# Kernel tuning notes

Hardware: AMD Instinct MI355X
Metric: run time of the kernel (lower is better)

The kernel has to match this reference:

```python
import jax, jax.numpy as jnp
import numpy as np

N, F_IN, H, C, E, K = 100000, 128, 512, 16, 3200000, 3
EPS = 1e-5


def setup_inputs() -> dict:
    key = jax.random.key(0)
    ks = jax.random.split(key, 12)
    x = jax.random.normal(ks[0], (N, F_IN), jnp.float32)
    edge_index = jax.random.randint(ks[1], (2, E), 0, N, jnp.int64)
    # TAGConv has K+1 hop linears (bias folded into one vector, like PyG)
    W1 = jax.random.normal(ks[2], (K + 1, F_IN, H), jnp.float32) * 0.02
    b1 = jnp.zeros((H,), jnp.float32)
    W2 = jax.random.normal(ks[3], (K + 1, H, H), jnp.float32) * 0.02
    b2 = jnp.zeros((H,), jnp.float32)
    W3 = jax.random.normal(ks[4], (K + 1, H, C), jnp.float32) * 0.02
    b3 = jnp.zeros((C,), jnp.float32)
    gn1_w = jnp.ones((H,), jnp.float32)
    gn1_b = jnp.zeros((H,), jnp.float32)
    gn1_a = jnp.ones((H,), jnp.float32)  # mean_scale alpha
    gn2_w = jnp.ones((H,), jnp.float32)
    gn2_b = jnp.zeros((H,), jnp.float32)
    gn2_a = jnp.ones((H,), jnp.float32)
    return {"x": x, "edge_index": edge_index,
            "W1": W1, "b1": b1, "W2": W2, "b2": b2, "W3": W3, "b3": b3,
            "gn1_w": gn1_w, "gn1_b": gn1_b, "gn1_a": gn1_a,
            "gn2_w": gn2_w, "gn2_b": gn2_b, "gn2_a": gn2_a}


def _gcn_norm(edge_index, n):
    # PyG TAGConv: gcn_norm with add_self_loops=False, all-ones edge weights
    row, col = edge_index[0], edge_index[1]  # source j, target i
    deg = jax.ops.segment_sum(jnp.ones((edge_index.shape[1],), jnp.float32), col,
                              num_segments=n)
    dinv = jnp.where(deg > 0, jax.lax.rsqrt(jnp.maximum(deg, 1.0)), 0.0)
    return row, col, dinv[row] * dinv[col]


def _prop(h, row, col, norm, n):
    # out[i] = sum_{(j->i)} norm_e * h[j]
    return jax.ops.segment_sum(norm[:, None] * h[row], col, num_segments=n)


def _tagconv(x, row, col, norm, W, b):
    n = x.shape[0]
    out = x @ W[0]
    h = x
    for k in range(1, W.shape[0]):
        h = _prop(h, row, col, norm, n)
        out = out + h @ W[k]
    return out + b


def _graphnorm(x, w, b, a):
    # single graph: per-graph mean/var over all nodes
    mean = jnp.mean(x, axis=0)
    sub = x - a * mean
    var = jnp.mean(sub * sub, axis=0)
    return sub * jax.lax.rsqrt(var + EPS) * w + b


def reference(x, edge_index, W1, b1, W2, b2, W3, b3,
              gn1_w, gn1_b, gn1_a, gn2_w, gn2_b, gn2_a):
    n = x.shape[0]
    row, col, norm = _gcn_norm(edge_index, n)
    h = jax.nn.relu(_tagconv(x, row, col, norm, W1, b1))
    h = _graphnorm(h, gn1_w, gn1_b, gn1_a)
    h = jax.nn.relu(_tagconv(h, row, col, norm, W2, b2))
    h = _graphnorm(h, gn2_w, gn2_b, gn2_a)
    return _tagconv(h, row, col, norm, W3, b3)
```

## Files before the change

kernel.cpp:

```cpp
#include <hip/hip_runtime.h>

#define NN 100000
#define EE 3200000
#define EPSF 1e-5f

typedef unsigned short u16;
typedef short bf16x8 __attribute__((ext_vector_type(8)));
typedef float f32x4 __attribute__((ext_vector_type(4)));

static inline int cdiv(int a, int b) { return (a + b - 1) / b; }

__device__ __forceinline__ float b2f(u16 u) {
    return __uint_as_float((unsigned int)u << 16);
}
__device__ __forceinline__ u16 f2b(float f) {
    unsigned int i = __float_as_uint(f);
    return (u16)((i + 0x7FFFu + ((i >> 16) & 1u)) >> 16);
}
__device__ __forceinline__ int ep_src(unsigned int p) { return (int)(p & 0x1FFFFu); }
__device__ __forceinline__ float ep_w(unsigned int p) {
    return __uint_as_float(p & 0xFFFE0000u);
}
__device__ __forceinline__ unsigned pkhi(float f0, float f1) {
    return __builtin_amdgcn_perm(__float_as_uint(f1), __float_as_uint(f0), 0x07060302u);
}

__global__ void k_init(int* __restrict__ deg, int* __restrict__ cursor,
                       float* __restrict__ stats) {
    int i = blockIdx.x * 256 + threadIdx.x;
    if (i < NN) {
        deg[i] = 0;
        cursor[i] = 0;
    }
    if (i < 2048) stats[i] = 0.f;
}

__global__ void k_deg(const int* __restrict__ col, int* __restrict__ deg) {
    int i = blockIdx.x * 256 + threadIdx.x;
    if (i < EE) atomicAdd(&deg[col[i]], 1);
}

__global__ void k_dinv(const int* __restrict__ deg, float* __restrict__ dinv) {
    int i = blockIdx.x * 256 + threadIdx.x;
    if (i < NN) {
        int d = deg[i];
        dinv[i] = d > 0 ? rsqrtf((float)d) : 0.f;
    }
}

__global__ void k_scan(const int* __restrict__ deg, int* __restrict__ offs) {
    __shared__ int sh[1024];
    int tid = threadIdx.x;
    int start = tid * 98;
    int end = min(start + 98, NN);
    int sum = 0;
    for (int i = start; i < end; ++i) sum += deg[i];
    sh[tid] = sum;
    __syncthreads();
    for (int off = 1; off < 1024; off <<= 1) {
        int t = (tid >= off) ? sh[tid - off] : 0;
        __syncthreads();
        sh[tid] += t;
        __syncthreads();
    }
    int base = tid ? sh[tid - 1] : 0;
    for (int i = start; i < end; ++i) {
        offs[i] = base;
        base += deg[i];
    }
    if (tid == 1023) offs[NN] = sh[1023];
}

__global__ void k_scatter(const int* __restrict__ row, const int* __restrict__ col,
                          const float* __restrict__ dinv, const int* __restrict__ offs,
                          int* __restrict__ cursor, unsigned int* __restrict__ ep) {
    int i = blockIdx.x * 256 + threadIdx.x;
    if (i < EE) {
        int c = col[i], r = row[i];
        int pos = offs[c] + atomicAdd(&cursor[c], 1);
        float w = dinv[r] * dinv[c];
        unsigned int u = __float_as_uint(w);
        unsigned int rb = (u + 0xFFFFu + ((u >> 17) & 1u)) & 0xFFFE0000u;
        ep[pos] = rb | (unsigned int)r;
    }
}

__global__ void k_cvt(const float* __restrict__ src, u16* __restrict__ dst, int n4) {
    int idx = blockIdx.x * 256 + threadIdx.x;
    if (idx >= n4) return;
    float4 v = ((const float4*)src)[idx];
    ushort4 o;
    o.x = f2b(v.x);
    o.y = f2b(v.y);
    o.z = f2b(v.z);
    o.w = f2b(v.w);
    ((ushort4*)dst)[idx] = o;
}

__global__ void k_cvt8s(const u16* __restrict__ src, int lds_, unsigned char* __restrict__ dst,
                        int ldd) {
    int idx = blockIdx.x * 256 + threadIdx.x;
    if (idx >= NN * 128) return;
    int node = idx >> 7, f2 = (idx & 127) << 1;
    ushort2 v = *(const ushort2*)(src + (size_t)node * lds_ + f2);
    int pk = __builtin_amdgcn_cvt_pk_fp8_f32(b2f(v.x), b2f(v.y), 0, false);
    uchar2 o;
    o.x = (unsigned char)(pk & 0xFF);
    o.y = (unsigned char)((pk >> 8) & 0xFF);
    *(uchar2*)(dst + (size_t)node * ldd + f2) = o;
}

template <int S8>
__global__ void k_prop_t(const void* __restrict__ in, int ldin,
                         unsigned char* __restrict__ out8, int ldo8,
                         const int* __restrict__ offs, const unsigned int* __restrict__ ep) {
    int node = blockIdx.x;
    int f2 = threadIdx.x << 1;
    int s = offs[node], e = offs[node + 1];
    const u16* inb = (const u16*)in;
    const unsigned char* in8 = (const unsigned char*)in;
    float a0 = 0.f, a1 = 0.f;
    int t = s;
    for (; t + 4 <= e; t += 4) {
        unsigned int p0 = ep[t], p1 = ep[t + 1], p2 = ep[t + 2], p3 = ep[t + 3];
        float x0, y0, x1, y1, x2, y2, x3, y3;
        if (S8) {
            uchar2 c0 = *(const uchar2*)(in8 + (size_t)ep_src(p0) * ldin + f2);
            uchar2 c1 = *(const uchar2*)(in8 + (size_t)ep_src(p1) * ldin + f2);
            uchar2 c2 = *(const uchar2*)(in8 + (size_t)ep_src(p2) * ldin + f2);
            uchar2 c3 = *(const uchar2*)(in8 + (size_t)ep_src(p3) * ldin + f2);
            int w0 = c0.x | (c0.y << 8), w1 = c1.x | (c1.y << 8);
            int w2 = c2.x | (c2.y << 8), w3 = c3.x | (c3.y << 8);
            x0 = __builtin_amdgcn_cvt_f32_fp8(w0, 0);
            y0 = __builtin_amdgcn_cvt_f32_fp8(w0, 1);
            x1 = __builtin_amdgcn_cvt_f32_fp8(w1, 0);
            y1 = __builtin_amdgcn_cvt_f32_fp8(w1, 1);
            x2 = __builtin_amdgcn_cvt_f32_fp8(w2, 0);
            y2 = __builtin_amdgcn_cvt_f32_fp8(w2, 1);
            x3 = __builtin_amdgcn_cvt_f32_fp8(w3, 0);
            y3 = __builtin_amdgcn_cvt_f32_fp8(w3, 1);
        } else {
            ushort2 v0 = *(const ushort2*)(inb + (size_t)ep_src(p0) * ldin + f2);
            ushort2 v1 = *(const ushort2*)(inb + (size_t)ep_src(p1) * ldin + f2);
            ushort2 v2 = *(const ushort2*)(inb + (size_t)ep_src(p2) * ldin + f2);
            ushort2 v3 = *(const ushort2*)(inb + (size_t)ep_src(p3) * ldin + f2);
            x0 = b2f(v0.x);
            y0 = b2f(v0.y);
            x1 = b2f(v1.x);
            y1 = b2f(v1.y);
            x2 = b2f(v2.x);
            y2 = b2f(v2.y);
            x3 = b2f(v3.x);
            y3 = b2f(v3.y);
        }
        float w0 = ep_w(p0), w1 = ep_w(p1), w2 = ep_w(p2), w3 = ep_w(p3);
        a0 = fmaf(w0, x0, a0);
        a1 = fmaf(w0, y0, a1);
        a0 = fmaf(w1, x1, a0);
        a1 = fmaf(w1, y1, a1);
        a0 = fmaf(w2, x2, a0);
        a1 = fmaf(w2, y2, a1);
        a0 = fmaf(w3, x3, a0);
        a1 = fmaf(w3, y3, a1);
    }
    for (; t < e; ++t) {
        unsigned int p0 = ep[t];
        float x0, y0;
        if (S8) {
            uchar2 c0 = *(const uchar2*)(in8 + (size_t)ep_src(p0) * ldin + f2);
            int w = c0.x | (c0.y << 8);
            x0 = __builtin_amdgcn_cvt_f32_fp8(w, 0);
            y0 = __builtin_amdgcn_cvt_f32_fp8(w, 1);
        } else {
            ushort2 v0 = *(const ushort2*)(inb + (size_t)ep_src(p0) * ldin + f2);
            x0 = b2f(v0.x);
            y0 = b2f(v0.y);
        }
        float w0 = ep_w(p0);
        a0 = fmaf(w0, x0, a0);
        a1 = fmaf(w0, y0, a1);
    }
    int pk = __builtin_amdgcn_cvt_pk_fp8_f32(a0, a1, 0, false);
    uchar2 o8;
    o8.x = (unsigned char)(pk & 0xFF);
    o8.y = (unsigned char)((pk >> 8) & 0xFF);
    *(uchar2*)(out8 + (size_t)node * ldo8 + f2) = o8;
}

__global__ void k_prop256(const unsigned char* __restrict__ in, int ldin,
                          unsigned char* __restrict__ out, int ldout,
                          const int* __restrict__ offs, const unsigned int* __restrict__ ep) {
    int node = blockIdx.x;
    int f4 = threadIdx.x << 2;
    int s = offs[node], e = offs[node + 1];
    float a0 = 0, a1 = 0, a2 = 0, a3 = 0;
    int t = s;
    for (; t + 4 <= e; t += 4) {
        unsigned int p[4];
        unsigned int v[4];
#pragma unroll
        for (int u = 0; u < 4; ++u) p[u] = ep[t + u];
#pragma unroll
        for (int u = 0; u < 4; ++u)
            v[u] = *(const unsigned int*)(in + (size_t)ep_src(p[u]) * ldin + f4);
#pragma unroll
        for (int u = 0; u < 4; ++u) {
            float w = ep_w(p[u]);
            a0 = fmaf(w, __builtin_amdgcn_cvt_f32_fp8((int)v[u], 0), a0);
            a1 = fmaf(w, __builtin_amdgcn_cvt_f32_fp8((int)v[u], 1), a1);
            a2 = fmaf(w, __builtin_amdgcn_cvt_f32_fp8((int)v[u], 2), a2);
            a3 = fmaf(w, __builtin_amdgcn_cvt_f32_fp8((int)v[u], 3), a3);
        }
    }
    for (; t < e; ++t) {
        unsigned int p0 = ep[t];
        unsigned int v = *(const unsigned int*)(in + (size_t)ep_src(p0) * ldin + f4);
        float w = ep_w(p0);
        a0 = fmaf(w, __builtin_amdgcn_cvt_f32_fp8((int)v, 0), a0);
        a1 = fmaf(w, __builtin_amdgcn_cvt_f32_fp8((int)v, 1), a1);
        a2 = fmaf(w, __builtin_amdgcn_cvt_f32_fp8((int)v, 2), a2);
        a3 = fmaf(w, __builtin_amdgcn_cvt_f32_fp8((int)v, 3), a3);
    }
    int p01 = __builtin_amdgcn_cvt_pk_fp8_f32(a0, a1, 0, false);
    int p23 = __builtin_amdgcn_cvt_pk_fp8_f32(a2, a3, 0, false);
    unsigned int o = (unsigned)(p01 & 0xFFFF) | ((unsigned)p23 << 16);
    *(unsigned int*)(out + (size_t)node * ldout + f4) = o;
}

__global__ void k_prop16(const float* __restrict__ in, int ldin,
                         const float* __restrict__ add, int ldadd,
                         float* __restrict__ out, const float* __restrict__ bias,
                         const int* __restrict__ offs, const unsigned int* __restrict__ ep) {
    int node = blockIdx.x * 16 + (threadIdx.x >> 4);
    if (node >= NN) return;
    int f = threadIdx.x & 15;
    float acc = add[(size_t)node * ldadd + f];
    int s = offs[node], e = offs[node + 1];
    int t = s;
    for (; t + 8 <= e; t += 8) {
        unsigned int p[8];
        float v[8];
#pragma unroll
        for (int u = 0; u < 8; ++u) p[u] = ep[t + u];
#pragma unroll
        for (int u = 0; u < 8; ++u) v[u] = in[(size_t)ep_src(p[u]) * ldin + f];
#pragma unroll
        for (int u = 0; u < 8; ++u) acc = fmaf(ep_w(p[u]), v[u], acc);
    }
    for (; t < e; ++t) {
        unsigned int p0 = ep[t];
        acc = fmaf(ep_w(p0), in[(size_t)ep_src(p0) * ldin + f], acc);
    }
    if (bias) acc += bias[f];
    out[node * 16 + f] = acc;
}

__device__ __forceinline__ void stage_bf16(char* lds, const char* src, size_t rowB,
                                           int colOff, int rowBase, int rowMax, int tid) {
    int wave = tid >> 6, lane = tid & 63;
#pragma unroll
    for (int i = 0; i < 2; ++i) {
        int L = i * 4096 + wave * 1024 + lane * 16;
        int r = L >> 6;
        int kog = (L & 63) ^ ((r & 3) << 4);
        int gr = rowBase + r;
        if (gr > rowMax) gr = rowMax;
        const char* g = src + (size_t)gr * rowB + colOff + kog;
        __builtin_amdgcn_global_load_lds(
            (const __attribute__((address_space(1))) void*)g,
            (__attribute__((address_space(3))) void*)(lds + i * 4096 + wave * 1024), 16, 0, 0);
    }
}

__global__ __launch_bounds__(256) void k_gemm_mfma(
    const void* __restrict__ A0, int lda0, const void* __restrict__ A1, int lda1,
    const void* __restrict__ A2, int lda2, const void* __restrict__ A3, int lda3, int a8mask,
    const u16* __restrict__ B0, const u16* __restrict__ B1, const u16* __restrict__ B2,
    const u16* __restrict__ B3, int ldb, void* __restrict__ Cv, int ldc, int M, int Ncols,
    int Ktot, int Kq, const float* __restrict__ bias, int relu, int cmode,
    float* __restrict__ statsOut) {
    __shared__ __align__(16) u16 As[128 * 32];
    __shared__ __align__(16) u16 Bs[128 * 32];
    __shared__ float sstat[256];
    char* AsB = (char*)As;
    char* BsB = (char*)Bs;
    int tid = threadIdx.x;
    int wave = tid >> 6, lane = tid & 63;
    int quad = lane >> 4, lq = lane & 15;
    int wr = wave >> 1, wc = wave & 1;
    int m0 = blockIdx.y * 128, n0 = blockIdx.x * 128;
    f32x4 acc[4][4] = {};
    if (statsOut) sstat[tid] = 0.f;

    int src = 0, kk = 0;
    for (int ks = 0; ks < Ktot; ks += 32) {
        const void* Ap = src == 0 ? A0 : src == 1 ? A1 : src == 2 ? A2 : A3;
        int lda = src == 0 ? lda0 : src == 1 ? lda1 : src == 2 ? lda2 : lda3;
        const u16* Bp = src == 0 ? B0 : src == 1 ? B1 : src == 2 ? B2 : B3;
        if ((a8mask >> src) & 1) {
            const unsigned char* A8 = (const unsigned char*)Ap;
            int r = tid >> 1, h = tid & 1;
            int gr = m0 + r;
            if (gr > M - 1) gr = M - 1;
            uint4 wv = *(const uint4*)(A8 + (size_t)gr * lda + kk + h * 16);
            uint4 lo, hi;
            lo.x = pkhi(__builtin_amdgcn_cvt_f32_fp8((int)wv.x, 0),
                        __builtin_amdgcn_cvt_f32_fp8((int)wv.x, 1));
            lo.y = pkhi(__builtin_amdgcn_cvt_f32_fp8((int)wv.x, 2),
                        __builtin_amdgcn_cvt_f32_fp8((int)wv.x, 3));
            lo.z = pkhi(__builtin_amdgcn_cvt_f32_fp8((int)wv.y, 0),
                        __builtin_amdgcn_cvt_f32_fp8((int)wv.y, 1));
            lo.w = pkhi(__builtin_amdgcn_cvt_f32_fp8((int)wv.y, 2),
                        __builtin_amdgcn_cvt_f32_fp8((int)wv.y, 3));
            hi.x = pkhi(__builtin_amdgcn_cvt_f32_fp8((int)wv.z, 0),
                        __builtin_amdgcn_cvt_f32_fp8((int)wv.z, 1));
            hi.y = pkhi(__builtin_amdgcn_cvt_f32_fp8((int)wv.z, 2),
                        __builtin_amdgcn_cvt_f32_fp8((int)wv.z, 3));
            hi.z = pkhi(__builtin_amdgcn_cvt_f32_fp8((int)wv.w, 0),
                        __builtin_amdgcn_cvt_f32_fp8((int)wv.w, 1));
            hi.w = pkhi(__builtin_amdgcn_cvt_f32_fp8((int)wv.w, 2),
                        __builtin_amdgcn_cvt_f32_fp8((int)wv.w, 3));
            int s = (r & 3) << 4;
            *(uint4*)(AsB + r * 64 + ((h * 32) ^ s)) = lo;
            *(uint4*)(AsB + r * 64 + ((h * 32 + 16) ^ s)) = hi;
        } else {
            stage_bf16(AsB, (const char*)Ap, (size_t)lda * 2, kk * 2, m0, M - 1, tid);
        }
        stage_bf16(BsB, (const char*)Bp, (size_t)ldb * 2, kk * 2, n0, Ncols - 1, tid);
        __syncthreads();
        bf16x8 af[4], bfr[4];
#pragma unroll
        for (int i = 0; i < 4; ++i) {
            int r = wr * 64 + i * 16 + lq;
            af[i] = *(bf16x8*)(AsB + r * 64 + ((quad * 16) ^ ((r & 3) << 4)));
        }
#pragma unroll
        for (int j = 0; j < 4; ++j) {
            int n = wc * 64 + j * 16 + lq;
            bfr[j] = *(bf16x8*)(BsB + n * 64 + ((quad * 16) ^ ((n & 3) << 4)));
        }
#pragma unroll
        for (int i = 0; i < 4; ++i)
#pragma unroll
            for (int j = 0; j < 4; ++j)
                acc[i][j] = __builtin_amdgcn_mfma_f32_16x16x32_bf16(af[i], bfr[j], acc[i][j],
                                                                    0, 0, 0);
        __syncthreads();
        kk += 32;
        if (kk == Kq) {
            kk = 0;
            ++src;
        }
    }

#pragma unroll
    for (int i = 0; i < 4; ++i) {
#pragma unroll
        for (int j = 0; j < 4; ++j) {
            int jc = wc * 64 + j * 16 + lq;
            int c = n0 + jc;
            bool cok = c < Ncols;
            float bcol = (bias && cok) ? bias[c] : 0.f;
            int rbase = m0 + wr * 64 + i * 16 + quad * 4;
            float ls = 0.f, lq2 = 0.f;
#pragma unroll
            for (int reg = 0; reg < 4; ++reg) {
                int r = rbase + reg;
                if (r >= M || !cok) continue;
                float t = acc[i][j][reg];
                if (cmode == 2) t += b2f(*((u16*)Cv + (size_t)r * ldc + c));
                t += bcol;
                if (relu) t = fmaxf(t, 0.f);
                if (cmode == 0)
                    ((float*)Cv)[(size_t)r * ldc + c] = t;
                else
                    *((u16*)Cv + (size_t)r * ldc + c) = f2b(t);
                ls += t;
                lq2 += t * t;
            }
            if (statsOut && cok) {
                atomicAdd(&sstat[jc], ls);
                atomicAdd(&sstat[128 + jc], lq2);
            }
        }
    }
    if (statsOut) {
        __syncthreads();
        if (tid < 128)
            atomicAdd(&statsOut[n0 + tid], sstat[tid]);
        else
            atomicAdd(&statsOut[512 + n0 + (tid - 128)], sstat[tid]);
    }
}

__global__ void k_gnorm(u16* __restrict__ X, int ld, const float* __restrict__ stats,
                        const float* __restrict__ w, const float* __restrict__ b,
                        const float* __restrict__ a) {
    int i = blockIdx.x;
    int c = threadIdx.x * 2;
    const float invn = 1.f / NN;
    ushort2 v = *(ushort2*)(X + (size_t)i * ld + c);
    float x0 = b2f(v.x), x1 = b2f(v.y);
    {
        float m = stats[c] * invn, q = stats[512 + c] * invn, al = a[c];
        float var = q - (2.f * al - al * al) * m * m;
        x0 = (x0 - al * m) * rsqrtf(var + EPSF) * w[c] + b[c];
    }
    {
        int c1 = c + 1;
        float m = stats[c1] * invn, q = stats[512 + c1] * invn, al = a[c1];
        float var = q - (2.f * al - al * al) * m * m;
        x1 = (x1 - al * m) * rsqrtf(var + EPSF) * w[c1] + b[c1];
    }
    v.x = f2b(x0);
    v.y = f2b(x1);
    *(ushort2*)(X + (size_t)i * ld + c) = v;
}

__global__ void k_wt(const float* __restrict__ src, u16* __restrict__ dst, int I, int O,
                     int total) {
    int idx = blockIdx.x * 256 + threadIdx.x;
    if (idx >= total) return;
    int io = I * O;
    int k = idx / io, rem = idx - k * io;
    int n = rem / I, i = rem - n * I;
    dst[idx] = f2b(src[(size_t)k * io + (size_t)i * O + n]);
}

__global__ void k_wt3(const float* __restrict__ W3, u16* __restrict__ W3T) {
    int idx = blockIdx.x * 256 + threadIdx.x;
    if (idx >= 64 * 512) return;
    int n = idx >> 9, i = idx & 511;
    int k = n >> 4, f = n & 15;
    W3T[idx] = f2b(W3[((size_t)k * 512 + i) * 16 + f]);
}

extern "C" void kernel_launch(void* const* d_in, const int* in_sizes, int n_in,
                              void* d_out, int out_size, void* d_ws, size_t ws_size,
                              hipStream_t stream) {
    const float* x = (const float*)d_in[0];
    const int* ei = (const int*)d_in[1];
    const float* W1 = (const float*)d_in[2];
    const float* b1 = (const float*)d_in[3];
    const float* W2 = (const float*)d_in[4];
    const float* b2 = (const float*)d_in[5];
    const float* W3 = (const float*)d_in[6];
    const float* b3 = (const float*)d_in[7];
    const float* g1w = (const float*)d_in[8];
    const float* g1b = (const float*)d_in[9];
    const float* g1a = (const float*)d_in[10];
    const float* g2w = (const float*)d_in[11];
    const float* g2b = (const float*)d_in[12];
    const float* g2a = (const float*)d_in[13];
    const int* row = ei;
    const int* col = ei + EE;

    char* p = (char*)d_ws;
    auto alloc = [&](size_t bytes) {
        char* r = p;
        p += (bytes + 255) & ~(size_t)255;
        return r;
    };
    u16* H1 = (u16*)alloc((size_t)NN * 512 * 2);
    u16* Y = (u16*)alloc((size_t)NN * 512 * 2);
    unsigned char* X8 = (unsigned char*)alloc((size_t)NN * 256);
    unsigned int* ep = (unsigned int*)alloc((size_t)EE * 4);
    u16* W1T = (u16*)alloc((size_t)4 * 512 * 128 * 2);
    u16* W2T = (u16*)alloc((size_t)4 * 512 * 512 * 2);
    u16* W3T = (u16*)alloc(64 * 512 * 2);
    float* dinv = (float*)alloc((size_t)NN * 4);
    float* stats = (float*)alloc(2048 * 4);
    int* deg = (int*)alloc((size_t)NN * 4);
    int* offs = (int*)alloc((size_t)(NN + 1) * 4);
    int* cursor = (int*)alloc((size_t)NN * 4);
    (void)ws_size;
    (void)in_sizes;
    (void)n_in;
    (void)out_size;

    u16* xb = Y;
    unsigned char* F8a = (unsigned char*)Y + (size_t)NN * 256;
    unsigned char* F8b = (unsigned char*)Y + (size_t)NN * 256 + (size_t)NN * 128;

    k_init<<<cdiv(NN, 256), 256, 0, stream>>>(deg, cursor, stats);
    k_deg<<<cdiv(EE, 256), 256, 0, stream>>>(col, deg);
    k_dinv<<<cdiv(NN, 256), 256, 0, stream>>>(deg, dinv);
    k_scan<<<1, 1024, 0, stream>>>(deg, offs);
    k_scatter<<<cdiv(EE, 256), 256, 0, stream>>>(row, col, dinv, offs, cursor, ep);
    k_wt<<<cdiv(4 * 128 * 512, 256), 256, 0, stream>>>(W1, W1T, 128, 512, 4 * 128 * 512);
    k_wt<<<cdiv(4 * 512 * 512, 256), 256, 0, stream>>>(W2, W2T, 512, 512, 4 * 512 * 512);
    k_wt3<<<cdiv(64 * 512, 256), 256, 0, stream>>>(W3, W3T);

    dim3 gg(512 / 128, cdiv(NN, 128));
    const size_t WQ = (size_t)512 * 512;
    const size_t W1Q = (size_t)512 * 128;

    k_cvt<<<cdiv(NN * 32, 256), 256, 0, stream>>>(x, xb, NN * 32);
    k_prop_t<0><<<NN, 64, 0, stream>>>(xb, 128, F8a, 128, offs, ep);
    k_gemm_mfma<<<gg, 256, 0, stream>>>(xb, 128, F8a, 128, xb, 128, xb, 128, 2, W1T,
                                        W1T + W1Q, W1T, W1T, 128, H1, 512, NN, 512, 256, 128,
                                        nullptr, 0, 1, nullptr);
    k_prop_t<1><<<NN, 64, 0, stream>>>(F8a, 128, F8b, 128, offs, ep);
    k_prop_t<1><<<NN, 64, 0, stream>>>(F8b, 128, F8a, 128, offs, ep);
    k_gemm_mfma<<<gg, 256, 0, stream>>>(F8b, 128, F8a, 128, xb, 128, xb, 128, 3,
                                        W1T + 2 * W1Q, W1T + 3 * W1Q, W1T, W1T, 128, H1, 512,
                                        NN, 512, 256, 128, b1, 1, 2, stats);
    k_gnorm<<<NN, 256, 0, stream>>>(H1, 512, stats, g1w, g1b, g1a);

    for (int c = 0; c < 2; ++c) {
        u16* h1c = H1 + 256 * c;
        k_cvt8s<<<cdiv(NN * 128, 256), 256, 0, stream>>>(h1c, 512, X8, 256);
        k_gemm_mfma<<<gg, 256, 0, stream>>>(h1c, 512, h1c, 512, h1c, 512, h1c, 512, 0,
                                            W2T + 256 * c, W2T, W2T, W2T, 512, Y, 512, NN, 512,
                                            256, 256, nullptr, 0, c == 0 ? 1 : 2, nullptr);
        unsigned char* hp1 = (unsigned char*)H1 + 512 * c;
        unsigned char* hp2 = hp1 + 256;
        k_prop256<<<NN, 64, 0, stream>>>(X8, 256, hp1, 1024, offs, ep);
        k_prop256<<<NN, 64, 0, stream>>>(hp1, 1024, hp2, 1024, offs, ep);
        k_prop256<<<NN, 64, 0, stream>>>(hp2, 1024, X8, 256, offs, ep);
        k_gemm_mfma<<<gg, 256, 0, stream>>>(hp1, 1024, hp2, 1024, X8, 256, X8, 256, 7,
                                            W2T + WQ + 256 * c, W2T + 2 * WQ + 256 * c,
                                            W2T + 3 * WQ + 256 * c, W2T, 512, Y, 512, NN, 512,
                                            768, 256, (c == 1) ? b2 : nullptr, c == 1 ? 1 : 0,
                                            2, (c == 1) ? (stats + 1024) : nullptr);
    }
    k_gnorm<<<NN, 256, 0, stream>>>(Y, 512, stats + 1024, g2w, g2b, g2a);

    float* G = (float*)H1;
    float* tA = (float*)X8;
    float* tB = tA + (size_t)NN * 16;
    {
        dim3 g3(1, cdiv(NN, 128));
        k_gemm_mfma<<<g3, 256, 0, stream>>>(Y, 512, Y, 512, Y, 512, Y, 512, 0, W3T, W3T, W3T,
                                            W3T, 512, G, 64, NN, 64, 512, 512, nullptr, 0, 0,
                                            nullptr);
    }
    k_prop16<<<cdiv(NN, 16), 256, 0, stream>>>(G + 48, 64, G + 32, 64, tA, nullptr, offs, ep);
    k_prop16<<<cdiv(NN, 16), 256, 0, stream>>>(tA, 16, G + 16, 64, tB, nullptr, offs, ep);
    k_prop16<<<cdiv(NN, 16), 256, 0, stream>>>(tB, 16, G + 0, 64, (float*)d_out, b3, offs, ep);
}
```

Baseline: 2.776 ms.

## Double-buffer GEMM LDS tiles, remap workgroups per XCD, merge hop GEMMs

The MFMA GEMM now uses double-buffered LDS. The next B tile is prefetched with global_load_lds and the next A tile is loaded into registers, with explicit waitcnts and one barrier per K step in place of two syncthreads. Blocks are remapped so consecutive tiles land on the same XCD, the LDS swizzle changes, and launch bounds request higher occupancy. On the host side, the layer-1 hop GEMMs and the second layer-2 chunk GEMMs are fused into single launches over all four hop sources. This cuts launches and the read-modify-write of the output, at the cost of more registers and LDS per block.

```diff
diff --git a/kernel.cpp b/kernel.cpp
--- a/kernel.cpp
+++ b/kernel.cpp
@@ -255,89 +255,134 @@
     out[node * 16 + f] = acc;
 }
 
-__device__ __forceinline__ void stage_bf16(char* lds, const char* src, size_t rowB,
-                                           int colOff, int rowBase, int rowMax, int tid) {
-    int wave = tid >> 6, lane = tid & 63;
-#pragma unroll
-    for (int i = 0; i < 2; ++i) {
-        int L = i * 4096 + wave * 1024 + lane * 16;
-        int r = L >> 6;
-        int kog = (L & 63) ^ ((r & 3) << 4);
-        int gr = rowBase + r;
-        if (gr > rowMax) gr = rowMax;
-        const char* g = src + (size_t)gr * rowB + colOff + kog;
-        __builtin_amdgcn_global_load_lds(
-            (const __attribute__((address_space(1))) void*)g,
-            (__attribute__((address_space(3))) void*)(lds + i * 4096 + wave * 1024), 16, 0, 0);
-    }
-}
-
-__global__ __launch_bounds__(256) void k_gemm_mfma(
+__global__ __launch_bounds__(256, 4) void k_gemm_mfma(
     const void* __restrict__ A0, int lda0, const void* __restrict__ A1, int lda1,
     const void* __restrict__ A2, int lda2, const void* __restrict__ A3, int lda3, int a8mask,
     const u16* __restrict__ B0, const u16* __restrict__ B1, const u16* __restrict__ B2,
     const u16* __restrict__ B3, int ldb, void* __restrict__ Cv, int ldc, int M, int Ncols,
     int Ktot, int Kq, const float* __restrict__ bias, int relu, int cmode,
     float* __restrict__ statsOut) {
-    __shared__ __align__(16) u16 As[128 * 32];
-    __shared__ __align__(16) u16 Bs[128 * 32];
+    __shared__ __align__(16) char AsB[2][8192];
+    __shared__ __align__(16) char BsB[2][8192];
     __shared__ float sstat[256];
-    char* AsB = (char*)As;
-    char* BsB = (char*)Bs;
     int tid = threadIdx.x;
     int wave = tid >> 6, lane = tid & 63;
     int quad = lane >> 4, lq = lane & 15;
     int wr = wave >> 1, wc = wave & 1;
-    int m0 = blockIdx.y * 128, n0 = blockIdx.x * 128;
+    int gx = gridDim.x;
+    int nwg = gx * (int)gridDim.y;
+    int lin = blockIdx.y * gx + blockIdx.x;
+    int xcd = lin & 7, kk8 = lin >> 3;
+    int q8 = nwg >> 3, r8 = nwg & 7;
+    int wgid = (xcd < r8 ? xcd * (q8 + 1) : r8 * (q8 + 1) + (xcd - r8) * q8) + kk8;
+    int m0 = (wgid / gx) * 128, n0 = (wgid % gx) * 128;
+    int r = tid >> 1, h = tid & 1;
+    int gr = m0 + r;
+    if (gr > M - 1) gr = M - 1;
     f32x4 acc[4][4] = {};
     if (statsOut) sstat[tid] = 0.f;
 
-    int src = 0, kk = 0;
-    for (int ks = 0; ks < Ktot; ks += 32) {
-        const void* Ap = src == 0 ? A0 : src == 1 ? A1 : src == 2 ? A2 : A3;
+    const int NT = Ktot >> 5;
+    const int spm = (Kq >> 5) - 1;
+    const int sps = __popc(spm);
+
+    auto loadA = [&](int u, uint4& x0, uint4& x1, int& t8) {
+        int sU = u < NT ? u : NT - 1;
+        int src = sU >> sps, kk = (sU & spm) << 5;
+        const char* Ap = (const char*)(src == 0 ? A0 : src == 1 ? A1 : src == 2 ? A2 : A3);
         int lda = src == 0 ? lda0 : src == 1 ? lda1 : src == 2 ? lda2 : lda3;
+        t8 = (a8mask >> src) & 1;
+        if (t8) {
+            x0 = *(const uint4*)(Ap + (size_t)gr * lda + kk + h * 16);
+        } else {
+            const char* base = Ap + (size_t)gr * ((size_t)lda * 2) + (size_t)kk * 2 + h * 32;
+            x0 = *(const uint4*)base;
+            x1 = *(const uint4*)(base + 16);
+        }
+    };
+    auto writeA = [&](int buf, uint4 x0, uint4 x1, int t8) {
+        uint4 lo, hi;
+        if (t8) {
+            lo.x = pkhi(__builtin_amdgcn_cvt_f32_fp8((int)x0.x, 0),
+                        __builtin_amdgcn_cvt_f32_fp8((int)x0.x, 1));
+            lo.y = pkhi(__builtin_amdgcn_cvt_f32_fp8((int)x0.x, 2),
+                        __builtin_amdgcn_cvt_f32_fp8((int)x0.x, 3));
+            lo.z = pkhi(__builtin_amdgcn_cvt_f32_fp8((int)x0.y, 0),
+                        __builtin_amdgcn_cvt_f32_fp8((int)x0.y, 1));
+            lo.w = pkhi(__builtin_amdgcn_cvt_f32_fp8((int)x0.y, 2),
+                        __builtin_amdgcn_cvt_f32_fp8((int)x0.y, 3));
+            hi.x = pkhi(__builtin_amdgcn_cvt_f32_fp8((int)x0.z, 0),
+                        __builtin_amdgcn_cvt_f32_fp8((int)x0.z, 1));
+            hi.y = pkhi(__builtin_amdgcn_cvt_f32_fp8((int)x0.z, 2),
+                        __builtin_amdgcn_cvt_f32_fp8((int)x0.z, 3));
+            hi.z = pkhi(__builtin_amdgcn_cvt_f32_fp8((int)x0.w, 0),
+                        __builtin_amdgcn_cvt_f32_fp8((int)x0.w, 1));
+            hi.w = pkhi(__builtin_amdgcn_cvt_f32_fp8((int)x0.w, 2),
+                        __builtin_amdgcn_cvt_f32_fp8((int)x0.w, 3));
+        } else {
+            lo = x0;
+            hi = x1;
+        }
+        int s = ((r >> 1) & 3) << 4;
+        char* dst = AsB[buf] + r * 64;
+        *(uint4*)(dst + ((h * 32) ^ s)) = lo;
+        *(uint4*)(dst + ((h * 32 + 16) ^ s)) = hi;
+    };
+    auto stageB = [&](int buf, int u) {
+        int sU = u < NT ? u : NT - 1;
+        int src = sU >> sps, kk = (sU & spm) << 5;
         const u16* Bp = src == 0 ? B0 : src == 1 ? B1 : src == 2 ? B2 : B3;
-        if ((a8mask >> src) & 1) {
-            const unsigned char* A8 = (const unsigned char*)Ap;
-            int r = tid >> 1, h = tid & 1;
-            int gr = m0 + r;
-            if (gr > M - 1) gr = M - 1;
-            uint4 wv = *(const uint4*)(A8 + (size_t)gr * lda + kk + h * 16);
-            uint4 lo, hi;
-            lo.x = pkhi(__builtin_amdgcn_cvt_f32_fp8((int)wv.x, 0),
-                        __builtin_amdgcn_cvt_f32_fp8((int)wv.x, 1));
-            lo.y = pkhi(__builtin_amdgcn_cvt_f32_fp8((int)wv.x, 2),
-                        __builtin_amdgcn_cvt_f32_fp8((int)wv.x, 3));
-            lo.z = pkhi(__builtin_amdgcn_cvt_f32_fp8((int)wv.y, 0),
-                        __builtin_amdgcn_cvt_f32_fp8((int)wv.y, 1));
-            lo.w = pkhi(__builtin_amdgcn_cvt_f32_fp8((int)wv.y, 2),
-                        __builtin_amdgcn_cvt_f32_fp8((int)wv.y, 3));
-            hi.x = pkhi(__builtin_amdgcn_cvt_f32_fp8((int)wv.z, 0),
-                        __builtin_amdgcn_cvt_f32_fp8((int)wv.z, 1));
-            hi.y = pkhi(__builtin_amdgcn_cvt_f32_fp8((int)wv.z, 2),
-                        __builtin_amdgcn_cvt_f32_fp8((int)wv.z, 3));
-            hi.z = pkhi(__builtin_amdgcn_cvt_f32_fp8((int)wv.w, 0),
-                        __builtin_amdgcn_cvt_f32_fp8((int)wv.w, 1));
-            hi.w = pkhi(__builtin_amdgcn_cvt_f32_fp8((int)wv.w, 2),
-                        __builtin_amdgcn_cvt_f32_fp8((int)wv.w, 3));
-            int s = (r & 3) << 4;
-            *(uint4*)(AsB + r * 64 + ((h * 32) ^ s)) = lo;
-            *(uint4*)(AsB + r * 64 + ((h * 32 + 16) ^ s)) = hi;
-        } else {
-            stage_bf16(AsB, (const char*)Ap, (size_t)lda * 2, kk * 2, m0, M - 1, tid);
-        }
-        stage_bf16(BsB, (const char*)Bp, (size_t)ldb * 2, kk * 2, n0, Ncols - 1, tid);
-        __syncthreads();
+#pragma unroll
+        for (int i = 0; i < 2; ++i) {
+            int L = i * 4096 + wave * 1024 + lane * 16;
+            int rr = L >> 6;
+            int kog = (L & 63) ^ (((rr >> 1) & 3) << 4);
+            int gn = n0 + rr;
+            if (gn > Ncols - 1) gn = Ncols - 1;
+            const char* g = (const char*)Bp + (size_t)gn * ((size_t)ldb * 2) +
+                            (size_t)kk * 2 + kog;
+            __builtin_amdgcn_global_load_lds(
+                (const __attribute__((address_space(1))) void*)g,
+                (__attribute__((address_space(3))) void*)(BsB[buf] + i * 4096 + wave * 1024),
+                16, 0, 0);
+        }
+    };
+
+    uint4 pa0, pa1;
+    int pt8;
+    {
+        uint4 a0_, a1_;
+        int t8_;
+        loadA(0, a0_, a1_, t8_);
+        stageB(0, 0);
+        asm volatile("s_waitcnt vmcnt(2)" ::: "memory");
+        __builtin_amdgcn_sched_barrier(0);
+        writeA(0, a0_, a1_, t8_);
+        loadA(1, pa0, pa1, pt8);
+        if (pt8)
+            asm volatile("s_waitcnt vmcnt(1) lgkmcnt(0)" ::: "memory");
+        else
+            asm volatile("s_waitcnt vmcnt(2) lgkmcnt(0)" ::: "memory");
+        __builtin_amdgcn_sched_barrier(0);
+        __builtin_amdgcn_s_barrier();
+    }
+
+    int cur = 0;
+    for (int t = 0; t < NT; ++t) {
+        int nxt = cur ^ 1;
+        stageB(nxt, t + 1);
+        const char* Ac = AsB[cur];
+        const char* Bc = BsB[cur];
         bf16x8 af[4], bfr[4];
 #pragma unroll
         for (int i = 0; i < 4; ++i) {
-            int r = wr * 64 + i * 16 + lq;
-            af[i] = *(bf16x8*)(AsB + r * 64 + ((quad * 16) ^ ((r & 3) << 4)));
+            int rr = wr * 64 + i * 16 + lq;
+            af[i] = *(const bf16x8*)(Ac + rr * 64 + ((quad * 16) ^ (((rr >> 1) & 3) << 4)));
         }
 #pragma unroll
         for (int j = 0; j < 4; ++j) {
-            int n = wc * 64 + j * 16 + lq;
-            bfr[j] = *(bf16x8*)(BsB + n * 64 + ((quad * 16) ^ ((n & 3) << 4)));
+            int nn2 = wc * 64 + j * 16 + lq;
+            bfr[j] = *(const bf16x8*)(Bc + nn2 * 64 + ((quad * 16) ^ (((nn2 >> 1) & 3) << 4)));
         }
 #pragma unroll
         for (int i = 0; i < 4; ++i)
@@ -345,12 +390,17 @@
             for (int j = 0; j < 4; ++j)
                 acc[i][j] = __builtin_amdgcn_mfma_f32_16x16x32_bf16(af[i], bfr[j], acc[i][j],
                                                                     0, 0, 0);
-        __syncthreads();
-        kk += 32;
-        if (kk == Kq) {
-            kk = 0;
-            ++src;
-        }
+        asm volatile("s_waitcnt vmcnt(2)" ::: "memory");
+        __builtin_amdgcn_sched_barrier(0);
+        writeA(nxt, pa0, pa1, pt8);
+        loadA(t + 2, pa0, pa1, pt8);
+        if (pt8)
+            asm volatile("s_waitcnt vmcnt(1) lgkmcnt(0)" ::: "memory");
+        else
+            asm volatile("s_waitcnt vmcnt(2) lgkmcnt(0)" ::: "memory");
+        __builtin_amdgcn_sched_barrier(0);
+        __builtin_amdgcn_s_barrier();
+        cur = nxt;
     }
 
 #pragma unroll
@@ -365,16 +415,16 @@
             float ls = 0.f, lq2 = 0.f;
 #pragma unroll
             for (int reg = 0; reg < 4; ++reg) {
-                int r = rbase + reg;
-                if (r >= M || !cok) continue;
+                int rr = rbase + reg;
+                if (rr >= M || !cok) continue;
                 float t = acc[i][j][reg];
-                if (cmode == 2) t += b2f(*((u16*)Cv + (size_t)r * ldc + c));
+                if (cmode == 2) t += b2f(*((u16*)Cv + (size_t)rr * ldc + c));
                 t += bcol;
                 if (relu) t = fmaxf(t, 0.f);
                 if (cmode == 0)
-                    ((float*)Cv)[(size_t)r * ldc + c] = t;
+                    ((float*)Cv)[(size_t)rr * ldc + c] = t;
                 else
-                    *((u16*)Cv + (size_t)r * ldc + c) = f2b(t);
+                    *((u16*)Cv + (size_t)rr * ldc + c) = f2b(t);
                 ls += t;
                 lq2 += t * t;
             }
@@ -497,32 +547,39 @@
 
     k_cvt<<<cdiv(NN * 32, 256), 256, 0, stream>>>(x, xb, NN * 32);
     k_prop_t<0><<<NN, 64, 0, stream>>>(xb, 128, F8a, 128, offs, ep);
-    k_gemm_mfma<<<gg, 256, 0, stream>>>(xb, 128, F8a, 128, xb, 128, xb, 128, 2, W1T,
-                                        W1T + W1Q, W1T, W1T, 128, H1, 512, NN, 512, 256, 128,
-                                        nullptr, 0, 1, nullptr);
     k_prop_t<1><<<NN, 64, 0, stream>>>(F8a, 128, F8b, 128, offs, ep);
-    k_prop_t<1><<<NN, 64, 0, stream>>>(F8b, 128, F8a, 128, offs, ep);
-    k_gemm_mfma<<<gg, 256, 0, stream>>>(F8b, 128, F8a, 128, xb, 128, xb, 128, 3,
-                                        W1T + 2 * W1Q, W1T + 3 * W1Q, W1T, W1T, 128, H1, 512,
-                                        NN, 512, 256, 128, b1, 1, 2, stats);
+    k_prop_t<1><<<NN, 64, 0, stream>>>(F8b, 128, X8, 128, offs, ep);
+    k_gemm_mfma<<<gg, 256, 0, stream>>>(xb, 128, F8a, 128, F8b, 128, X8, 128, 14, W1T,
+                                        W1T + W1Q, W1T + 2 * W1Q, W1T + 3 * W1Q, 128, H1, 512,
+                                        NN, 512, 512, 128, b1, 1, 1, stats);
     k_gnorm<<<NN, 256, 0, stream>>>(H1, 512, stats, g1w, g1b, g1a);
 
-    for (int c = 0; c < 2; ++c) {
-        u16* h1c = H1 + 256 * c;
-        k_cvt8s<<<cdiv(NN * 128, 256), 256, 0, stream>>>(h1c, 512, X8, 256);
-        k_gemm_mfma<<<gg, 256, 0, stream>>>(h1c, 512, h1c, 512, h1c, 512, h1c, 512, 0,
-                                            W2T + 256 * c, W2T, W2T, W2T, 512, Y, 512, NN, 512,
-                                            256, 256, nullptr, 0, c == 0 ? 1 : 2, nullptr);
-        unsigned char* hp1 = (unsigned char*)H1 + 512 * c;
-        unsigned char* hp2 = hp1 + 256;
-        k_prop256<<<NN, 64, 0, stream>>>(X8, 256, hp1, 1024, offs, ep);
-        k_prop256<<<NN, 64, 0, stream>>>(hp1, 1024, hp2, 1024, offs, ep);
-        k_prop256<<<NN, 64, 0, stream>>>(hp2, 1024, X8, 256, offs, ep);
-        k_gemm_mfma<<<gg, 256, 0, stream>>>(hp1, 1024, hp2, 1024, X8, 256, X8, 256, 7,
-                                            W2T + WQ + 256 * c, W2T + 2 * WQ + 256 * c,
-                                            W2T + 3 * WQ + 256 * c, W2T, 512, Y, 512, NN, 512,
-                                            768, 256, (c == 1) ? b2 : nullptr, c == 1 ? 1 : 0,
-                                            2, (c == 1) ? (stats + 1024) : nullptr);
+    unsigned char* hpA = (unsigned char*)H1;
+    unsigned char* hpB = (unsigned char*)H1 + 256;
+    {
+        u16* h1c0 = H1;
+        k_cvt8s<<<cdiv(NN * 128, 256), 256, 0, stream>>>(h1c0, 512, X8, 256);
+        k_gemm_mfma<<<gg, 256, 0, stream>>>(h1c0, 512, h1c0, 512, h1c0, 512, h1c0, 512, 0,
+                                            W2T, W2T, W2T, W2T, 512, Y, 512, NN, 512, 256,
+                                            256, nullptr, 0, 1, nullptr);
+        k_prop256<<<NN, 64, 0, stream>>>(X8, 256, hpA, 1024, offs, ep);
+        k_prop256<<<NN, 64, 0, stream>>>(hpA, 1024, hpB, 1024, offs, ep);
+        k_prop256<<<NN, 64, 0, stream>>>(hpB, 1024, X8, 256, offs, ep);
+        k_gemm_mfma<<<gg, 256, 0, stream>>>(hpA, 1024, hpB, 1024, X8, 256, X8, 256, 7,
+                                            W2T + WQ, W2T + 2 * WQ, W2T + 3 * WQ, W2T, 512,
+                                            Y, 512, NN, 512, 768, 256, nullptr, 0, 2,
+                                            nullptr);
+    }
+    {
+        u16* h1c1 = H1 + 256;
+        k_cvt8s<<<cdiv(NN * 128, 256), 256, 0, stream>>>(h1c1, 512, X8, 256);
+        k_prop256<<<NN, 64, 0, stream>>>(X8, 256, hpA, 1024, offs, ep);
+        k_prop256<<<NN, 64, 0, stream>>>(hpA, 1024, hpB, 1024, offs, ep);
+        k_prop256<<<NN, 64, 0, stream>>>(hpB, 1024, X8, 256, offs, ep);
+        k_gemm_mfma<<<gg, 256, 0, stream>>>(h1c1, 512, hpA, 1024, hpB, 1024, X8, 256, 14,
+                                            W2T + 256, W2T + WQ + 256, W2T + 2 * WQ + 256,
+                                            W2T + 3 * WQ + 256, 512, Y, 512, NN, 512, 1024,
+                                            256, b2, 1, 2, stats + 1024);
     }
     k_gnorm<<<NN, 256, 0, stream>>>(Y, 512, stats + 1024, g2w, g2b, g2a);
 
```

New measurement: 2.988 ms. 1.08x slower.

## Merge TAGConv hop GEMMs into fewer launches, remap workgroups per XCD, widen LDS swizzle

Applied to the files above, without the earlier changes.

Layer 1 now runs all three propagations first and does a single K=512 GEMM over four sources (x and three hops), writing the output once instead of two GEMM passes with a read-modify-write. The second half of layer 2 folds its hop-0 GEMM into the hop GEMM so that half needs one launch. The GEMM kernel also remaps block IDs so consecutive tiles land on the same XCD for L2 locality, replaces the running src/kk counters with shift/mask math, and changes the LDS XOR swizzle to use (r>>1)&3 to reduce bank conflicts. Together these cut GEMM launches and the extra read/write of the bf16 output. The cost is needing an extra fp8 buffer (X8) live during layer 1, and the K-index math assumes Kq is a power of two.

```diff
diff --git a/kernel.cpp b/kernel.cpp
--- a/kernel.cpp
+++ b/kernel.cpp
@@ -262,7 +262,7 @@
     for (int i = 0; i < 2; ++i) {
         int L = i * 4096 + wave * 1024 + lane * 16;
         int r = L >> 6;
-        int kog = (L & 63) ^ ((r & 3) << 4);
+        int kog = (L & 63) ^ (((r >> 1) & 3) << 4);
         int gr = rowBase + r;
         if (gr > rowMax) gr = rowMax;
         const char* g = src + (size_t)gr * rowB + colOff + kog;
@@ -279,21 +279,29 @@
     const u16* __restrict__ B3, int ldb, void* __restrict__ Cv, int ldc, int M, int Ncols,
     int Ktot, int Kq, const float* __restrict__ bias, int relu, int cmode,
     float* __restrict__ statsOut) {
-    __shared__ __align__(16) u16 As[128 * 32];
-    __shared__ __align__(16) u16 Bs[128 * 32];
+    __shared__ __align__(16) char AsB[8192];
+    __shared__ __align__(16) char BsB[8192];
     __shared__ float sstat[256];
-    char* AsB = (char*)As;
-    char* BsB = (char*)Bs;
     int tid = threadIdx.x;
     int wave = tid >> 6, lane = tid & 63;
     int quad = lane >> 4, lq = lane & 15;
     int wr = wave >> 1, wc = wave & 1;
-    int m0 = blockIdx.y * 128, n0 = blockIdx.x * 128;
+    int gx = gridDim.x;
+    int nwg = gx * (int)gridDim.y;
+    int lin = blockIdx.y * gx + blockIdx.x;
+    int xcd = lin & 7, k8 = lin >> 3;
+    int q8 = nwg >> 3, r8 = nwg & 7;
+    int wgid = (xcd < r8 ? xcd * (q8 + 1) : r8 * (q8 + 1) + (xcd - r8) * q8) + k8;
+    int m0 = (wgid / gx) * 128, n0 = (wgid % gx) * 128;
     f32x4 acc[4][4] = {};
     if (statsOut) sstat[tid] = 0.f;
 
-    int src = 0, kk = 0;
-    for (int ks = 0; ks < Ktot; ks += 32) {
+    const int NT = Ktot >> 5;
+    const int spm = (Kq >> 5) - 1;
+    const int sps = __popc(spm);
+
+    for (int t = 0; t < NT; ++t) {
+        int src = t >> sps, kk = (t & spm) << 5;
         const void* Ap = src == 0 ? A0 : src == 1 ? A1 : src == 2 ? A2 : A3;
         int lda = src == 0 ? lda0 : src == 1 ? lda1 : src == 2 ? lda2 : lda3;
         const u16* Bp = src == 0 ? B0 : src == 1 ? B1 : src == 2 ? B2 : B3;
@@ -320,9 +328,10 @@
                         __builtin_amdgcn_cvt_f32_fp8((int)wv.w, 1));
             hi.w = pkhi(__builtin_amdgcn_cvt_f32_fp8((int)wv.w, 2),
                         __builtin_amdgcn_cvt_f32_fp8((int)wv.w, 3));
-            int s = (r & 3) << 4;
-            *(uint4*)(AsB + r * 64 + ((h * 32) ^ s)) = lo;
-            *(uint4*)(AsB + r * 64 + ((h * 32 + 16) ^ s)) = hi;
+            int s = ((r >> 1) & 3) << 4;
+            char* dst = AsB + r * 64;
+            *(uint4*)(dst + ((h * 32) ^ s)) = lo;
+            *(uint4*)(dst + ((h * 32 + 16) ^ s)) = hi;
         } else {
             stage_bf16(AsB, (const char*)Ap, (size_t)lda * 2, kk * 2, m0, M - 1, tid);
         }
@@ -331,13 +340,13 @@
         bf16x8 af[4], bfr[4];
 #pragma unroll
         for (int i = 0; i < 4; ++i) {
-            int r = wr * 64 + i * 16 + lq;
-            af[i] = *(bf16x8*)(AsB + r * 64 + ((quad * 16) ^ ((r & 3) << 4)));
+            int rr = wr * 64 + i * 16 + lq;
+            af[i] = *(const bf16x8*)(AsB + rr * 64 + ((quad * 16) ^ (((rr >> 1) & 3) << 4)));
         }
 #pragma unroll
         for (int j = 0; j < 4; ++j) {
-            int n = wc * 64 + j * 16 + lq;
-            bfr[j] = *(bf16x8*)(BsB + n * 64 + ((quad * 16) ^ ((n & 3) << 4)));
+            int nn2 = wc * 64 + j * 16 + lq;
+            bfr[j] = *(const bf16x8*)(BsB + nn2 * 64 + ((quad * 16) ^ (((nn2 >> 1) & 3) << 4)));
         }
 #pragma unroll
         for (int i = 0; i < 4; ++i)
@@ -346,11 +355,6 @@
                 acc[i][j] = __builtin_amdgcn_mfma_f32_16x16x32_bf16(af[i], bfr[j], acc[i][j],
                                                                     0, 0, 0);
         __syncthreads();
-        kk += 32;
-        if (kk == Kq) {
-            kk = 0;
-            ++src;
-        }
     }
 
 #pragma unroll
@@ -365,16 +369,16 @@
             float ls = 0.f, lq2 = 0.f;
 #pragma unroll
             for (int reg = 0; reg < 4; ++reg) {
-                int r = rbase + reg;
-                if (r >= M || !cok) continue;
+                int rr = rbase + reg;
+                if (rr >= M || !cok) continue;
                 float t = acc[i][j][reg];
-                if (cmode == 2) t += b2f(*((u16*)Cv + (size_t)r * ldc + c));
+                if (cmode == 2) t += b2f(*((u16*)Cv + (size_t)rr * ldc + c));
                 t += bcol;
                 if (relu) t = fmaxf(t, 0.f);
                 if (cmode == 0)
-                    ((float*)Cv)[(size_t)r * ldc + c] = t;
+                    ((float*)Cv)[(size_t)rr * ldc + c] = t;
                 else
-                    *((u16*)Cv + (size_t)r * ldc + c) = f2b(t);
+                    *((u16*)Cv + (size_t)rr * ldc + c) = f2b(t);
                 ls += t;
                 lq2 += t * t;
             }
@@ -497,32 +501,39 @@
 
     k_cvt<<<cdiv(NN * 32, 256), 256, 0, stream>>>(x, xb, NN * 32);
     k_prop_t<0><<<NN, 64, 0, stream>>>(xb, 128, F8a, 128, offs, ep);
-    k_gemm_mfma<<<gg, 256, 0, stream>>>(xb, 128, F8a, 128, xb, 128, xb, 128, 2, W1T,
-                                        W1T + W1Q, W1T, W1T, 128, H1, 512, NN, 512, 256, 128,
-                                        nullptr, 0, 1, nullptr);
     k_prop_t<1><<<NN, 64, 0, stream>>>(F8a, 128, F8b, 128, offs, ep);
-    k_prop_t<1><<<NN, 64, 0, stream>>>(F8b, 128, F8a, 128, offs, ep);
-    k_gemm_mfma<<<gg, 256, 0, stream>>>(F8b, 128, F8a, 128, xb, 128, xb, 128, 3,
-                                        W1T + 2 * W1Q, W1T + 3 * W1Q, W1T, W1T, 128, H1, 512,
-                                        NN, 512, 256, 128, b1, 1, 2, stats);
+    k_prop_t<1><<<NN, 64, 0, stream>>>(F8b, 128, X8, 128, offs, ep);
+    k_gemm_mfma<<<gg, 256, 0, stream>>>(xb, 128, F8a, 128, F8b, 128, X8, 128, 14, W1T,
+                                        W1T + W1Q, W1T + 2 * W1Q, W1T + 3 * W1Q, 128, H1, 512,
+                                        NN, 512, 512, 128, b1, 1, 1, stats);
     k_gnorm<<<NN, 256, 0, stream>>>(H1, 512, stats, g1w, g1b, g1a);
 
-    for (int c = 0; c < 2; ++c) {
-        u16* h1c = H1 + 256 * c;
-        k_cvt8s<<<cdiv(NN * 128, 256), 256, 0, stream>>>(h1c, 512, X8, 256);
-        k_gemm_mfma<<<gg, 256, 0, stream>>>(h1c, 512, h1c, 512, h1c, 512, h1c, 512, 0,
-                                            W2T + 256 * c, W2T, W2T, W2T, 512, Y, 512, NN, 512,
-                                            256, 256, nullptr, 0, c == 0 ? 1 : 2, nullptr);
-        unsigned char* hp1 = (unsigned char*)H1 + 512 * c;
-        unsigned char* hp2 = hp1 + 256;
-        k_prop256<<<NN, 64, 0, stream>>>(X8, 256, hp1, 1024, offs, ep);
-        k_prop256<<<NN, 64, 0, stream>>>(hp1, 1024, hp2, 1024, offs, ep);
-        k_prop256<<<NN, 64, 0, stream>>>(hp2, 1024, X8, 256, offs, ep);
-        k_gemm_mfma<<<gg, 256, 0, stream>>>(hp1, 1024, hp2, 1024, X8, 256, X8, 256, 7,
-                                            W2T + WQ + 256 * c, W2T + 2 * WQ + 256 * c,
-                                            W2T + 3 * WQ + 256 * c, W2T, 512, Y, 512, NN, 512,
-                                            768, 256, (c == 1) ? b2 : nullptr, c == 1 ? 1 : 0,
-                                            2, (c == 1) ? (stats + 1024) : nullptr);
+    unsigned char* hpA = (unsigned char*)H1;
+    unsigned char* hpB = (unsigned char*)H1 + 256;
+    {
+        u16* h1c0 = H1;
+        k_cvt8s<<<cdiv(NN * 128, 256), 256, 0, stream>>>(h1c0, 512, X8, 256);
+        k_gemm_mfma<<<gg, 256, 0, stream>>>(h1c0, 512, h1c0, 512, h1c0, 512, h1c0, 512, 0,
+                                            W2T, W2T, W2T, W2T, 512, Y, 512, NN, 512, 256,
+                                            256, nullptr, 0, 1, nullptr);
+        k_prop256<<<NN, 64, 0, stream>>>(X8, 256, hpA, 1024, offs, ep);
+        k_prop256<<<NN, 64, 0, stream>>>(hpA, 1024, hpB, 1024, offs, ep);
+        k_prop256<<<NN, 64, 0, stream>>>(hpB, 1024, X8, 256, offs, ep);
+        k_gemm_mfma<<<gg, 256, 0, stream>>>(hpA, 1024, hpB, 1024, X8, 256, X8, 256, 7,
+                                            W2T + WQ, W2T + 2 * WQ, W2T + 3 * WQ, W2T, 512,
+                                            Y, 512, NN, 512, 768, 256, nullptr, 0, 2,
+                                            nullptr);
+    }
+    {
+        u16* h1c1 = H1 + 256;
+        k_cvt8s<<<cdiv(NN * 128, 256), 256, 0, stream>>>(h1c1, 512, X8, 256);
+        k_prop256<<<NN, 64, 0, stream>>>(X8, 256, hpA, 1024, offs, ep);
+        k_prop256<<<NN, 64, 0, stream>>>(hpA, 1024, hpB, 1024, offs, ep);
+        k_prop256<<<NN, 64, 0, stream>>>(hpB, 1024, X8, 256, offs, ep);
+        k_gemm_mfma<<<gg, 256, 0, stream>>>(h1c1, 512, hpA, 1024, hpB, 1024, X8, 256, 14,
+                                            W2T + 256, W2T + WQ + 256, W2T + 2 * WQ + 256,
+                                            W2T + 3 * WQ + 256, 512, Y, 512, NN, 512, 1024,
+                                            256, b2, 1, 2, stats + 1024);
     }
     k_gnorm<<<NN, 256, 0, stream>>>(Y, 512, stats + 1024, g2w, g2b, g2a);
 
```

Measured after the change: 2.565 ms. 7.6% less time.
